# Kernel optimization log

Measured on AMD Instinct MI355X. Metric: run time of the kernel, lower is better.

## Reference

```python
import jax, jax.numpy as jnp
import numpy as np

B, H, S, D = 4, 16, 2048, 128

def setup_inputs() -> dict:
    key = jax.random.key(0)
    kq, kk, kv = jax.random.split(key, 3)
    Q = jax.random.normal(kq, (B, H, S, D), dtype=jnp.float32)
    K = jax.random.normal(kk, (B, H, S, D), dtype=jnp.float32)
    V = jax.random.normal(kv, (B, H, S, D), dtype=jnp.float32)
    # causal mask: True = attend (lower triangle incl. diagonal)
    mask = jnp.tril(jnp.ones((S, S), dtype=jnp.bool_))[None, None, :, :]
    return {"Q": Q, "K": K, "V": V, "mask": mask}

def reference(Q, K, V, mask):
    d_k = Q.shape[-1]
    scale = 1.0 / jnp.sqrt(jnp.asarray(d_k, Q.dtype))
    # [B,H,Sq,Sk] score matrix (naive, materialized, as in the original)
    scores = jnp.einsum('bhqd,bhkd->bhqk', Q, K) * scale
    scores = jnp.where(mask, scores, jnp.asarray(-1e9, scores.dtype))
    attn = jax.nn.softmax(scores, axis=-1)
    return jnp.einsum('bhqk,bhkd->bhqd', attn, V)
```

## Files before the change

kernel.cpp:

```cpp
#include <hip/hip_runtime.h>
#include <hip/hip_bf16.h>

constexpr int S_LEN = 2048;
constexpr int D_DIM = 128;
constexpr int NBH   = 64;
constexpr int NKT   = 32;
constexpr size_t TILE_SHORTS = 64 * 128;
constexpr size_t PAIR_SHORTS = 2 * TILE_SHORTS;
constexpr size_t WS_NEEDED   = (size_t)NBH * NKT * PAIR_SHORTS * 2;

typedef __attribute__((ext_vector_type(8))) short short8;
typedef __attribute__((ext_vector_type(4))) float f32x4;

__device__ __forceinline__ short f2bf(float f) {
    unsigned u = __builtin_bit_cast(unsigned, f);
    u += 0x7fffu + ((u >> 16) & 1u);
    return (short)(u >> 16);
}

__device__ __forceinline__ int kpos(int dc, int key) { return dc ^ (key & 15); }
__device__ __forceinline__ int vpos(int kc, int d) {
    return kc ^ ((d >> 3) & 7) ^ (d & 7);
}

__global__ __launch_bounds__(256)
void preprocess_kv(const float* __restrict__ K, const float* __restrict__ V,
                   short* __restrict__ ws) {
    __shared__ short sv[128 * 64];
    const int tid = threadIdx.x;
    const int kt  = blockIdx.x;
    const int bh  = blockIdx.y;
    const size_t inbase = ((size_t)bh * S_LEN + (size_t)kt * 64) * D_DIM;
    short* wk = ws + ((size_t)bh * NKT + kt) * PAIR_SHORTS;
    short* wv = wk + TILE_SHORTS;

    for (int it = 0; it < 4; ++it) {
        const int idx = (it * 256 + tid) * 8;
        const int key = idx >> 7, d = idx & 127;
        const float* kp = K + inbase + (size_t)key * D_DIM + d;
        float4 a = *reinterpret_cast<const float4*>(kp);
        float4 b = *reinterpret_cast<const float4*>(kp + 4);
        short8 f;
        f[0]=f2bf(a.x); f[1]=f2bf(a.y); f[2]=f2bf(a.z); f[3]=f2bf(a.w);
        f[4]=f2bf(b.x); f[5]=f2bf(b.y); f[6]=f2bf(b.z); f[7]=f2bf(b.w);
        *reinterpret_cast<short8*>(&wk[key * 128 + (kpos(d >> 3, key) << 3)]) = f;
        const float* vp = V + inbase + (size_t)key * D_DIM + d;
        float4 c = *reinterpret_cast<const float4*>(vp);
        float4 e = *reinterpret_cast<const float4*>(vp + 4);
        float vals[8] = {c.x,c.y,c.z,c.w,e.x,e.y,e.z,e.w};
        for (int j = 0; j < 8; ++j) {
            const int dr = d + j;
            sv[dr * 64 + (vpos(key >> 3, dr) << 3) + (key & 7)] = f2bf(vals[j]);
        }
    }
    __syncthreads();
    for (int it = 0; it < 4; ++it) {
        const int off = (it * 256 + tid) * 8;
        *reinterpret_cast<short8*>(&wv[off]) =
            *reinterpret_cast<const short8*>(&sv[off]);
    }
}

__device__ __forceinline__ void async_copy_1k(const short* gsrc, short* ldst,
                                              int lane) {
    __builtin_amdgcn_global_load_lds(
        (const __attribute__((address_space(1))) void*)(gsrc + lane * 8),
        (__attribute__((address_space(3))) void*)ldst, 16, 0, 0);
}
__device__ __forceinline__ void dma_tile16k(const short* gsrc, short* ldst,
                                            int wid, int lane) {
    for (int i = 0; i < 4; ++i) {
        const int s = wid * 4 + i;
        async_copy_1k(gsrc + s * 512, ldst + s * 512, lane);
    }
}

__global__ __launch_bounds__(256, 4)
void fa_causal_main(const float* __restrict__ Q, const short* __restrict__ ws,
                    float* __restrict__ Out) {
    __shared__ short sK [64 * 128];
    __shared__ short sVt[128 * 64];
    __shared__ short sP [64 * 64];

    const int tid  = threadIdx.x;
    const int wid  = tid >> 6;
    const int lane = tid & 63;
    const int quad = lane >> 4;
    const int l16  = lane & 15;

    const int x  = blockIdx.x;
    const int bh = blockIdx.y;
    const size_t base = (size_t)bh * S_LEN * D_DIM;
    const short* tiles = ws + (size_t)bh * NKT * PAIR_SHORTS;
    const float scale = 0.08838834764831845f;

    for (int pi = 0; pi < 2; ++pi) {
        const int qt = (pi == 0) ? (31 - x) : x;
        const int q0 = qt * 64;

        float4 qa[4], qb[4];
        {
            const float* qp = Q + base + (size_t)(q0 + wid * 16 + l16) * D_DIM;
            for (int kk = 0; kk < 4; ++kk) {
                const int d0 = kk * 32 + quad * 8;
                qa[kk] = *reinterpret_cast<const float4*>(qp + d0);
                qb[kk] = *reinterpret_cast<const float4*>(qp + d0 + 4);
            }
        }
        dma_tile16k(tiles, sK, wid, lane);
        dma_tile16k(tiles + TILE_SHORTS, sVt, wid, lane);

        short8 q_frag[4];
        for (int kk = 0; kk < 4; ++kk) {
            short8 f;
            f[0]=f2bf(qa[kk].x*scale); f[1]=f2bf(qa[kk].y*scale);
            f[2]=f2bf(qa[kk].z*scale); f[3]=f2bf(qa[kk].w*scale);
            f[4]=f2bf(qb[kk].x*scale); f[5]=f2bf(qb[kk].y*scale);
            f[6]=f2bf(qb[kk].z*scale); f[7]=f2bf(qb[kk].w*scale);
            q_frag[kk] = f;
        }

        f32x4 o_acc[8];
        for (int i = 0; i < 8; ++i) o_acc[i] = f32x4{0.f,0.f,0.f,0.f};
        float m_i[4], l_i[4];
        for (int r = 0; r < 4; ++r) { m_i[r] = -1e30f; l_i[r] = 0.f; }

        for (int kt = 0; kt <= qt; ++kt) {
            asm volatile("s_waitcnt vmcnt(4) lgkmcnt(0)" ::: "memory");
            __builtin_amdgcn_s_barrier();
            asm volatile("" ::: "memory");

            f32x4 s_acc[4];
            for (int ct = 0; ct < 4; ++ct) {
                const int key = ct * 16 + l16;
                f32x4 acc = f32x4{0.f,0.f,0.f,0.f};
                for (int kk = 0; kk < 4; ++kk) {
                    short8 kf = *reinterpret_cast<const short8*>(
                        &sK[key * 128 + (kpos(kk * 4 + quad, key) << 3)]);
                    acc = __builtin_amdgcn_mfma_f32_16x16x32_bf16(q_frag[kk], kf, acc, 0, 0, 0);
                }
                s_acc[ct] = acc;
            }

            if (kt == qt) {
                for (int ct = 0; ct < 4; ++ct) {
                    const int kg = ct * 16 + l16;
                    for (int r = 0; r < 4; ++r)
                        if (kg > wid * 16 + quad * 4 + r) s_acc[ct][r] = -1e30f;
                }
            }

            float tm[4];
            for (int r = 0; r < 4; ++r)
                tm[r] = fmaxf(fmaxf(s_acc[0][r], s_acc[1][r]),
                              fmaxf(s_acc[2][r], s_acc[3][r]));
            for (int off = 1; off < 16; off <<= 1)
                for (int r = 0; r < 4; ++r)
                    tm[r] = fmaxf(tm[r], __shfl_xor(tm[r], off));
            float alpha[4], m_new[4], rs[4];
            for (int r = 0; r < 4; ++r) {
                m_new[r] = fmaxf(m_i[r], tm[r]);
                alpha[r] = __expf(m_i[r] - m_new[r]);
                rs[r] = 0.f;
            }
            for (int ct = 0; ct < 4; ++ct)
                for (int r = 0; r < 4; ++r) {
                    float p = __expf(s_acc[ct][r] - m_new[r]);
                    s_acc[ct][r] = p;
                    rs[r] += p;
                }
            for (int off = 1; off < 16; off <<= 1)
                for (int r = 0; r < 4; ++r)
                    rs[r] += __shfl_xor(rs[r], off);
            for (int r = 0; r < 4; ++r) {
                l_i[r] = alpha[r] * l_i[r] + rs[r];
                m_i[r] = m_new[r];
            }
            for (int nt = 0; nt < 8; ++nt)
                for (int r = 0; r < 4; ++r)
                    o_acc[nt][r] *= alpha[r];

            __syncthreads();

            if (kt < qt)
                dma_tile16k(tiles + (size_t)(kt + 1) * PAIR_SHORTS, sK, wid, lane);

            for (int ct = 0; ct < 4; ++ct)
                for (int r = 0; r < 4; ++r) {
                    const int row = wid * 16 + quad * 4 + r;
                    const int col = ct * 16 + l16;
                    sP[row * 64 + (((col >> 3) ^ (row & 7)) << 3) + (col & 7)]
                        = f2bf(s_acc[ct][r]);
                }

            {
                const int prow = wid * 16 + l16;
                short8 pf[2];
                for (int k2 = 0; k2 < 2; ++k2)
                    pf[k2] = *reinterpret_cast<const short8*>(
                        &sP[prow * 64 + (((k2 * 4 + quad) ^ (prow & 7)) << 3)]);
                for (int nt = 0; nt < 8; ++nt) {
                    const int vrow = nt * 16 + l16;
                    for (int k2 = 0; k2 < 2; ++k2) {
                        short8 vf = *reinterpret_cast<const short8*>(
                            &sVt[vrow * 64 + (vpos(k2 * 4 + quad, vrow) << 3)]);
                        o_acc[nt] = __builtin_amdgcn_mfma_f32_16x16x32_bf16(pf[k2], vf, o_acc[nt], 0, 0, 0);
                    }
                }
            }

            asm volatile("s_waitcnt lgkmcnt(0)" ::: "memory");
            __builtin_amdgcn_s_barrier();
            asm volatile("" ::: "memory");

            if (kt < qt)
                dma_tile16k(tiles + (size_t)(kt + 1) * PAIR_SHORTS + TILE_SHORTS,
                            sVt, wid, lane);
        }

        for (int nt = 0; nt < 8; ++nt)
            for (int r = 0; r < 4; ++r) {
                const int qrow = q0 + wid * 16 + quad * 4 + r;
                Out[base + (size_t)qrow * D_DIM + nt * 16 + l16] = o_acc[nt][r] / l_i[r];
            }
    }
}

constexpr int SK_STRIDE  = 136;
constexpr int SVT_STRIDE = 72;
constexpr int SP_STRIDE  = 72;

__global__ __launch_bounds__(256, 4)
void fa_causal_fallback(const float* __restrict__ Q, const float* __restrict__ K,
                        const float* __restrict__ V, float* __restrict__ Out) {
    __shared__ short sK[64 * SK_STRIDE];
    __shared__ short sVt[128 * SVT_STRIDE];
    short* sP = sK;
    const int tid  = threadIdx.x;
    const int wid  = tid >> 6;
    const int lane = tid & 63;
    const int quad = lane >> 4;
    const int l16  = lane & 15;
    const int x  = blockIdx.x;
    const int bh = blockIdx.y;
    const size_t base = (size_t)bh * S_LEN * D_DIM;
    const float scale = 0.08838834764831845f;
    for (int pi = 0; pi < 2; ++pi) {
        const int qt = (pi == 0) ? (31 - x) : x;
        const int q0 = qt * 64;
        short8 q_frag[4];
        {
            const float* qp = Q + base + (size_t)(q0 + wid * 16 + l16) * D_DIM;
            for (int kk = 0; kk < 4; ++kk) {
                const int d0 = kk * 32 + quad * 8;
                float4 a = *reinterpret_cast<const float4*>(qp + d0);
                float4 b = *reinterpret_cast<const float4*>(qp + d0 + 4);
                short8 f;
                f[0]=f2bf(a.x*scale); f[1]=f2bf(a.y*scale);
                f[2]=f2bf(a.z*scale); f[3]=f2bf(a.w*scale);
                f[4]=f2bf(b.x*scale); f[5]=f2bf(b.y*scale);
                f[6]=f2bf(b.z*scale); f[7]=f2bf(b.w*scale);
                q_frag[kk] = f;
            }
        }
        f32x4 o_acc[8];
        for (int i = 0; i < 8; ++i) o_acc[i] = f32x4{0.f,0.f,0.f,0.f};
        float m_i[4], l_i[4];
        for (int r = 0; r < 4; ++r) { m_i[r] = -1e30f; l_i[r] = 0.f; }
        for (int kt = 0; kt <= qt; ++kt) {
            for (int it = 0; it < 4; ++it) {
                const int idx = (it * 256 + tid) * 8;
                const int key = idx >> 7, d = idx & 127;
                const float* kp = K + base + (size_t)(kt * 64 + key) * D_DIM + d;
                float4 a = *reinterpret_cast<const float4*>(kp);
                float4 b = *reinterpret_cast<const float4*>(kp + 4);
                short8 f;
                f[0]=f2bf(a.x); f[1]=f2bf(a.y); f[2]=f2bf(a.z); f[3]=f2bf(a.w);
                f[4]=f2bf(b.x); f[5]=f2bf(b.y); f[6]=f2bf(b.z); f[7]=f2bf(b.w);
                *reinterpret_cast<short8*>(&sK[key * SK_STRIDE + d]) = f;
            }
            for (int it = 0; it < 4; ++it) {
                const int idx = (it * 256 + tid) * 8;
                const int key = idx >> 7, d = idx & 127;
                const int kc = key >> 3, kw = key & 7;
                const float* vp = V + base + (size_t)(kt * 64 + key) * D_DIM + d;
                float4 a = *reinterpret_cast<const float4*>(vp);
                float4 b = *reinterpret_cast<const float4*>(vp + 4);
                float vals[8] = {a.x,a.y,a.z,a.w,b.x,b.y,b.z,b.w};
                const int rc = (d >> 3) & 7;
                const int cs = (kc ^ rc) * 8 + kw;
                for (int j = 0; j < 8; ++j)
                    sVt[(d + j) * SVT_STRIDE + cs] = f2bf(vals[j]);
            }
            __syncthreads();
            f32x4 s_acc[4];
            for (int ct = 0; ct < 4; ++ct) {
                f32x4 acc = f32x4{0.f,0.f,0.f,0.f};
                for (int kk = 0; kk < 4; ++kk) {
                    short8 kf = *reinterpret_cast<const short8*>(
                        &sK[(ct * 16 + l16) * SK_STRIDE + kk * 32 + quad * 8]);
                    acc = __builtin_amdgcn_mfma_f32_16x16x32_bf16(q_frag[kk], kf, acc, 0, 0, 0);
                }
                s_acc[ct] = acc;
            }
            if (kt == qt) {
                for (int ct = 0; ct < 4; ++ct) {
                    const int kg = ct * 16 + l16;
                    for (int r = 0; r < 4; ++r)
                        if (kg > wid * 16 + quad * 4 + r) s_acc[ct][r] = -1e30f;
                }
            }
            float tm[4];
            for (int r = 0; r < 4; ++r)
                tm[r] = fmaxf(fmaxf(s_acc[0][r], s_acc[1][r]),
                              fmaxf(s_acc[2][r], s_acc[3][r]));
            for (int off = 1; off < 16; off <<= 1)
                for (int r = 0; r < 4; ++r)
                    tm[r] = fmaxf(tm[r], __shfl_xor(tm[r], off));
            float alpha[4], m_new[4], rs[4];
            for (int r = 0; r < 4; ++r) {
                m_new[r] = fmaxf(m_i[r], tm[r]);
                alpha[r] = __expf(m_i[r] - m_new[r]);
                rs[r] = 0.f;
            }
            for (int ct = 0; ct < 4; ++ct)
                for (int r = 0; r < 4; ++r) {
                    float p = __expf(s_acc[ct][r] - m_new[r]);
                    s_acc[ct][r] = p;
                    rs[r] += p;
                }
            for (int off = 1; off < 16; off <<= 1)
                for (int r = 0; r < 4; ++r)
                    rs[r] += __shfl_xor(rs[r], off);
            for (int r = 0; r < 4; ++r) {
                l_i[r] = alpha[r] * l_i[r] + rs[r];
                m_i[r] = m_new[r];
            }
            for (int nt = 0; nt < 8; ++nt)
                for (int r = 0; r < 4; ++r)
                    o_acc[nt][r] *= alpha[r];
            __syncthreads();
            for (int ct = 0; ct < 4; ++ct)
                for (int r = 0; r < 4; ++r) {
                    const int row = wid * 16 + quad * 4 + r;
                    const int col = ct * 16 + l16;
                    sP[row * SP_STRIDE + (((col >> 3) ^ ((row >> 2) & 7)) << 3) + (col & 7)]
                        = f2bf(s_acc[ct][r]);
                }
            {
                const int prow = wid * 16 + l16;
                const int pxr  = (prow >> 2) & 7;
                for (int nt = 0; nt < 8; ++nt) {
                    const int vrow = nt * 16 + l16;
                    const int vxr  = (vrow >> 3) & 7;
                    for (int k2 = 0; k2 < 2; ++k2) {
                        const int chunk = k2 * 4 + quad;
                        short8 pf = *reinterpret_cast<const short8*>(
                            &sP[prow * SP_STRIDE + ((chunk ^ pxr) << 3)]);
                        short8 vf = *reinterpret_cast<const short8*>(
                            &sVt[vrow * SVT_STRIDE + ((chunk ^ vxr) << 3)]);
                        o_acc[nt] = __builtin_amdgcn_mfma_f32_16x16x32_bf16(pf, vf, o_acc[nt], 0, 0, 0);
                    }
                }
            }
            __syncthreads();
        }
        for (int nt = 0; nt < 8; ++nt)
            for (int r = 0; r < 4; ++r) {
                const int qrow = q0 + wid * 16 + quad * 4 + r;
                Out[base + (size_t)qrow * D_DIM + nt * 16 + l16] = o_acc[nt][r] / l_i[r];
            }
    }
}

extern "C" void kernel_launch(void* const* d_in, const int* in_sizes, int n_in,
                              void* d_out, int out_size, void* d_ws, size_t ws_size,
                              hipStream_t stream) {
    const float* Q = (const float*)d_in[0];
    const float* K = (const float*)d_in[1];
    const float* V = (const float*)d_in[2];
    float* Out = (float*)d_out;

    if (ws_size >= WS_NEEDED) {
        short* ws = (short*)d_ws;
        preprocess_kv<<<dim3(NKT, NBH), 256, 0, stream>>>(K, V, ws);
        fa_causal_main<<<dim3(16, NBH), 256, 0, stream>>>(Q, ws, Out);
    } else {
        fa_causal_fallback<<<dim3(16, NBH), 256, 0, stream>>>(Q, K, V, Out);
    }
}
```

Before: 422.7 us.

## Process 128-row query tiles per block so K/V tiles serve twice the rows

Each block now handles a single 128-row query tile, with each wave owning two 16-row sub-tiles, in place of two 64-row tiles processed one after the other. Every loaded K/V tile in shared memory is reused by twice as many query rows, which halves the global-to-LDS traffic per unit of work. The block-to-work mapping is remapped, with heaviest tiles first and bh interleaved across the grid. In exchange, register pressure and LDS use grow (occupancy hint lowered from 4 to 3), there are fewer blocks, and the grid shape must match the new 16-wide linear mapping (launch code not shown).

```diff
diff --git a/kernel.cpp b/kernel.cpp
--- a/kernel.cpp
+++ b/kernel.cpp
@@ -75,12 +75,12 @@
     }
 }
 
-__global__ __launch_bounds__(256, 4)
+__global__ __launch_bounds__(256, 3)
 void fa_causal_main(const float* __restrict__ Q, const short* __restrict__ ws,
                     float* __restrict__ Out) {
     __shared__ short sK [64 * 128];
     __shared__ short sVt[128 * 64];
-    __shared__ short sP [64 * 64];
+    __shared__ short sP [128 * 64];
 
     const int tid  = threadIdx.x;
     const int wid  = tid >> 6;
@@ -88,47 +88,62 @@
     const int quad = lane >> 4;
     const int l16  = lane & 15;
 
-    const int x  = blockIdx.x;
-    const int bh = blockIdx.y;
+    const int L   = blockIdx.x + (blockIdx.y << 4);
+    const int bh  = ((L & 7) << 3) | ((L >> 3) & 7);
+    const int qt  = 15 - (L >> 6);
+    const int q0  = qt * 128;
+    const int kend = 2 * qt + 2;
+
     const size_t base = (size_t)bh * S_LEN * D_DIM;
     const short* tiles = ws + (size_t)bh * NKT * PAIR_SHORTS;
     const float scale = 0.08838834764831845f;
 
-    for (int pi = 0; pi < 2; ++pi) {
-        const int qt = (pi == 0) ? (31 - x) : x;
-        const int q0 = qt * 64;
-
-        float4 qa[4], qb[4];
-        {
-            const float* qp = Q + base + (size_t)(q0 + wid * 16 + l16) * D_DIM;
-            for (int kk = 0; kk < 4; ++kk) {
-                const int d0 = kk * 32 + quad * 8;
-                qa[kk] = *reinterpret_cast<const float4*>(qp + d0);
-                qb[kk] = *reinterpret_cast<const float4*>(qp + d0 + 4);
-            }
-        }
-        dma_tile16k(tiles, sK, wid, lane);
-        dma_tile16k(tiles + TILE_SHORTS, sVt, wid, lane);
-
-        short8 q_frag[4];
+    float4 qa[2][4], qb[2][4];
+    #pragma unroll
+    for (int mh = 0; mh < 2; ++mh) {
+        const float* qp = Q + base +
+            (size_t)(q0 + wid * 32 + mh * 16 + l16) * D_DIM;
+        for (int kk = 0; kk < 4; ++kk) {
+            const int d0 = kk * 32 + quad * 8;
+            qa[mh][kk] = *reinterpret_cast<const float4*>(qp + d0);
+            qb[mh][kk] = *reinterpret_cast<const float4*>(qp + d0 + 4);
+        }
+    }
+    dma_tile16k(tiles, sK, wid, lane);
+    dma_tile16k(tiles + TILE_SHORTS, sVt, wid, lane);
+
+    short8 q_frag[2][4];
+    #pragma unroll
+    for (int mh = 0; mh < 2; ++mh)
         for (int kk = 0; kk < 4; ++kk) {
             short8 f;
-            f[0]=f2bf(qa[kk].x*scale); f[1]=f2bf(qa[kk].y*scale);
-            f[2]=f2bf(qa[kk].z*scale); f[3]=f2bf(qa[kk].w*scale);
-            f[4]=f2bf(qb[kk].x*scale); f[5]=f2bf(qb[kk].y*scale);
-            f[6]=f2bf(qb[kk].z*scale); f[7]=f2bf(qb[kk].w*scale);
-            q_frag[kk] = f;
-        }
-
-        f32x4 o_acc[8];
-        for (int i = 0; i < 8; ++i) o_acc[i] = f32x4{0.f,0.f,0.f,0.f};
-        float m_i[4], l_i[4];
-        for (int r = 0; r < 4; ++r) { m_i[r] = -1e30f; l_i[r] = 0.f; }
-
-        for (int kt = 0; kt <= qt; ++kt) {
-            asm volatile("s_waitcnt vmcnt(4) lgkmcnt(0)" ::: "memory");
-            __builtin_amdgcn_s_barrier();
-            asm volatile("" ::: "memory");
+            f[0]=f2bf(qa[mh][kk].x*scale); f[1]=f2bf(qa[mh][kk].y*scale);
+            f[2]=f2bf(qa[mh][kk].z*scale); f[3]=f2bf(qa[mh][kk].w*scale);
+            f[4]=f2bf(qb[mh][kk].x*scale); f[5]=f2bf(qb[mh][kk].y*scale);
+            f[6]=f2bf(qb[mh][kk].z*scale); f[7]=f2bf(qb[mh][kk].w*scale);
+            q_frag[mh][kk] = f;
+        }
+
+    f32x4 o_acc[2][8];
+    #pragma unroll
+    for (int mh = 0; mh < 2; ++mh)
+        for (int i = 0; i < 8; ++i) o_acc[mh][i] = f32x4{0.f,0.f,0.f,0.f};
+    float m_i[2][4], l_i[2][4];
+    #pragma unroll
+    for (int mh = 0; mh < 2; ++mh)
+        for (int r = 0; r < 4; ++r) { m_i[mh][r] = -1e30f; l_i[mh][r] = 0.f; }
+
+    for (int kt = 0; kt < kend; ++kt) {
+        asm volatile("s_waitcnt vmcnt(4) lgkmcnt(0)" ::: "memory");
+        __builtin_amdgcn_s_barrier();
+        asm volatile("" ::: "memory");
+
+        const int kb = kt * 64;
+
+        #pragma unroll
+        for (int mh = 0; mh < 2; ++mh) {
+            const int rmin = q0 + wid * 32 + mh * 16;
+            if (kb > rmin + 15) continue;
 
             f32x4 s_acc[4];
             for (int ct = 0; ct < 4; ++ct) {
@@ -137,16 +152,16 @@
                 for (int kk = 0; kk < 4; ++kk) {
                     short8 kf = *reinterpret_cast<const short8*>(
                         &sK[key * 128 + (kpos(kk * 4 + quad, key) << 3)]);
-                    acc = __builtin_amdgcn_mfma_f32_16x16x32_bf16(q_frag[kk], kf, acc, 0, 0, 0);
+                    acc = __builtin_amdgcn_mfma_f32_16x16x32_bf16(q_frag[mh][kk], kf, acc, 0, 0, 0);
                 }
                 s_acc[ct] = acc;
             }
 
-            if (kt == qt) {
+            if (kb + 63 > rmin) {
                 for (int ct = 0; ct < 4; ++ct) {
-                    const int kg = ct * 16 + l16;
+                    const int kg = kb + ct * 16 + l16;
                     for (int r = 0; r < 4; ++r)
-                        if (kg > wid * 16 + quad * 4 + r) s_acc[ct][r] = -1e30f;
+                        if (kg > rmin + quad * 4 + r) s_acc[ct][r] = -1e30f;
                 }
             }
 
@@ -159,8 +174,8 @@
                     tm[r] = fmaxf(tm[r], __shfl_xor(tm[r], off));
             float alpha[4], m_new[4], rs[4];
             for (int r = 0; r < 4; ++r) {
-                m_new[r] = fmaxf(m_i[r], tm[r]);
-                alpha[r] = __expf(m_i[r] - m_new[r]);
+                m_new[r] = fmaxf(m_i[mh][r], tm[r]);
+                alpha[r] = __expf(m_i[mh][r] - m_new[r]);
                 rs[r] = 0.f;
             }
             for (int ct = 0; ct < 4; ++ct)
@@ -173,57 +188,72 @@
                 for (int r = 0; r < 4; ++r)
                     rs[r] += __shfl_xor(rs[r], off);
             for (int r = 0; r < 4; ++r) {
-                l_i[r] = alpha[r] * l_i[r] + rs[r];
-                m_i[r] = m_new[r];
+                l_i[mh][r] = alpha[r] * l_i[mh][r] + rs[r];
+                m_i[mh][r] = m_new[r];
             }
             for (int nt = 0; nt < 8; ++nt)
                 for (int r = 0; r < 4; ++r)
-                    o_acc[nt][r] *= alpha[r];
-
-            __syncthreads();
-
-            if (kt < qt)
-                dma_tile16k(tiles + (size_t)(kt + 1) * PAIR_SHORTS, sK, wid, lane);
+                    o_acc[mh][nt][r] *= alpha[r];
 
             for (int ct = 0; ct < 4; ++ct)
                 for (int r = 0; r < 4; ++r) {
-                    const int row = wid * 16 + quad * 4 + r;
+                    const int row = wid * 32 + mh * 16 + quad * 4 + r;
                     const int col = ct * 16 + l16;
                     sP[row * 64 + (((col >> 3) ^ (row & 7)) << 3) + (col & 7)]
                         = f2bf(s_acc[ct][r]);
                 }
-
-            {
-                const int prow = wid * 16 + l16;
-                short8 pf[2];
+        }
+
+        __syncthreads();
+
+        if (kt + 1 < kend)
+            dma_tile16k(tiles + (size_t)(kt + 1) * PAIR_SHORTS, sK, wid, lane);
+
+        {
+            const bool act0 = (kb <= q0 + wid * 32 + 15);
+            const bool act1 = (kb <= q0 + wid * 32 + 16 + 15);
+            const int pr0 = wid * 32 + l16;
+            const int pr1 = wid * 32 + 16 + l16;
+            short8 pf0[2], pf1[2];
+            if (act0)
                 for (int k2 = 0; k2 < 2; ++k2)
-                    pf[k2] = *reinterpret_cast<const short8*>(
-                        &sP[prow * 64 + (((k2 * 4 + quad) ^ (prow & 7)) << 3)]);
-                for (int nt = 0; nt < 8; ++nt) {
-                    const int vrow = nt * 16 + l16;
-                    for (int k2 = 0; k2 < 2; ++k2) {
-                        short8 vf = *reinterpret_cast<const short8*>(
-                            &sVt[vrow * 64 + (vpos(k2 * 4 + quad, vrow) << 3)]);
-                        o_acc[nt] = __builtin_amdgcn_mfma_f32_16x16x32_bf16(pf[k2], vf, o_acc[nt], 0, 0, 0);
-                    }
-                }
-            }
-
-            asm volatile("s_waitcnt lgkmcnt(0)" ::: "memory");
-            __builtin_amdgcn_s_barrier();
-            asm volatile("" ::: "memory");
-
-            if (kt < qt)
-                dma_tile16k(tiles + (size_t)(kt + 1) * PAIR_SHORTS + TILE_SHORTS,
-                            sVt, wid, lane);
-        }
-
-        for (int nt = 0; nt < 8; ++nt)
-            for (int r = 0; r < 4; ++r) {
-                const int qrow = q0 + wid * 16 + quad * 4 + r;
-                Out[base + (size_t)qrow * D_DIM + nt * 16 + l16] = o_acc[nt][r] / l_i[r];
-            }
-    }
+                    pf0[k2] = *reinterpret_cast<const short8*>(
+                        &sP[pr0 * 64 + (((k2 * 4 + quad) ^ (pr0 & 7)) << 3)]);
+            if (act1)
+                for (int k2 = 0; k2 < 2; ++k2)
+                    pf1[k2] = *reinterpret_cast<const short8*>(
+                        &sP[pr1 * 64 + (((k2 * 4 + quad) ^ (pr1 & 7)) << 3)]);
+            for (int nt = 0; nt < 8; ++nt) {
+                const int vrow = nt * 16 + l16;
+                for (int k2 = 0; k2 < 2; ++k2) {
+                    short8 vf = *reinterpret_cast<const short8*>(
+                        &sVt[vrow * 64 + (vpos(k2 * 4 + quad, vrow) << 3)]);
+                    if (act0)
+                        o_acc[0][nt] = __builtin_amdgcn_mfma_f32_16x16x32_bf16(pf0[k2], vf, o_acc[0][nt], 0, 0, 0);
+                    if (act1)
+                        o_acc[1][nt] = __builtin_amdgcn_mfma_f32_16x16x32_bf16(pf1[k2], vf, o_acc[1][nt], 0, 0, 0);
+                }
+            }
+        }
+
+        asm volatile("s_waitcnt lgkmcnt(0)" ::: "memory");
+        __builtin_amdgcn_s_barrier();
+        asm volatile("" ::: "memory");
+
+        if (kt + 1 < kend)
+            dma_tile16k(tiles + (size_t)(kt + 1) * PAIR_SHORTS + TILE_SHORTS,
+                        sVt, wid, lane);
+    }
+
+    #pragma unroll
+    for (int mh = 0; mh < 2; ++mh)
+        for (int r = 0; r < 4; ++r) {
+            const float inv = 1.0f / l_i[mh][r];
+            const int qrow = q0 + wid * 32 + mh * 16 + quad * 4 + r;
+            float* op = Out + base + (size_t)qrow * D_DIM;
+            for (int nt = 0; nt < 8; ++nt)
+                op[nt * 16 + l16] = o_acc[mh][nt][r] * inv;
+        }
 }
 
 constexpr int SK_STRIDE  = 136;
```

New measurement: 754.3 us. +78.4%, slower.
